# Kernel tuning notes

Measured on AMD Instinct MI355X. Metric: run time of the kernel, lower is better.

The kernel has to match this reference:

```python
import jax, jax.numpy as jnp
import numpy as np

D_MODEL = 1024
N_HEADS = 16
D_K = D_MODEL // N_HEADS


def setup_inputs() -> dict:
    key = jax.random.key(0)
    ks = jax.random.split(key, 9)
    s = 1.0 / np.sqrt(D_MODEL)
    inp = {
        "x": jax.random.normal(ks[0], (2, 2048, D_MODEL), dtype=jnp.float32),
        "wq": jax.random.uniform(ks[1], (D_MODEL, D_MODEL), jnp.float32, -s, s),
        "bq": jax.random.uniform(ks[2], (D_MODEL,), jnp.float32, -s, s),
        "wk": jax.random.uniform(ks[3], (D_MODEL, D_MODEL), jnp.float32, -s, s),
        "bk": jax.random.uniform(ks[4], (D_MODEL,), jnp.float32, -s, s),
        "wv": jax.random.uniform(ks[5], (D_MODEL, D_MODEL), jnp.float32, -s, s),
        "bv": jax.random.uniform(ks[6], (D_MODEL,), jnp.float32, -s, s),
        "wo": jax.random.uniform(ks[7], (D_MODEL, D_MODEL), jnp.float32, -s, s),
        "bo": jax.random.uniform(ks[8], (D_MODEL,), jnp.float32, -s, s),
    }
    return inp


def reference(x, wq, bq, wk, bk, wv, bv, wo, bo):
    B, S, _ = x.shape
    # projections; weights stored as [in, out] (torch Linear applies x @ W^T; here W pre-transposed)
    def proj(w, b):
        y = x @ w + b  # [B,S,D]
        return y.reshape(B, S, N_HEADS, D_K).transpose(0, 2, 1, 3)  # [B,H,S,dk]
    q, k, v = proj(wq, bq), proj(wk, bk), proj(wv, bv)
    scores = jnp.einsum('bhqd,bhkd->bhqk', q, k) / jnp.sqrt(jnp.float32(D_K))
    attn = jax.nn.softmax(scores, axis=-1)  # dropout p=0 -> identity
    ctx = jnp.einsum('bhqk,bhkd->bhqd', attn, v)
    ctx = ctx.transpose(0, 2, 1, 3).reshape(B, S, D_MODEL)
    return ctx @ wo + bo
```

## Files before the change

### kernel.cpp

```cpp
#include <hip/hip_runtime.h>
#include <hip/hip_bf16.h>
#include <math.h>


typedef __attribute__((ext_vector_type(8))) short bf8v;
typedef __attribute__((ext_vector_type(4))) float f32x4;
typedef __attribute__((ext_vector_type(16))) float f32x16;

#define mfma32(a, b, c) __builtin_amdgcn_mfma_f32_32x32x16_bf16((a), (b), (c), 0, 0, 0)

constexpr int Dm = 1024;
constexpr int NH = 16;
constexpr int DK = 64;
constexpr int BB = 2;
constexpr int SS = 2048;
constexpr int MM = BB * SS;

__device__ __forceinline__ unsigned short f2bf(float f) {
  union { float f; unsigned u; } v; v.f = f;
  unsigned r = v.u + 0x7fffu + ((v.u >> 16) & 1u);
  return (unsigned short)(r >> 16);
}

__device__ __forceinline__ unsigned cvt_pk_bf16(float lo, float hi) {
  unsigned r;
  asm("v_cvt_pk_bf16_f32 %0, %1, %2" : "=v"(r) : "v"(lo), "v"(hi));
  return r;
}

__device__ __forceinline__ void swap32(unsigned &a, unsigned &b) {
  asm("v_permlane32_swap_b32 %0, %1" : "+v"(a), "+v"(b));
}

__device__ __forceinline__ void gl_lds16(const void* g, void* l) {
  __builtin_amdgcn_global_load_lds(
      (const __attribute__((address_space(1))) void*)g,
      (__attribute__((address_space(3))) void*)l, 16, 0, 0);
}

__device__ __forceinline__ int swz4(int r) { return (r ^ (r >> 2)) & 3; }
__device__ __forceinline__ bf8v frag4(const unsigned short* base, int R, int s0) {
  return *(const bf8v*)((const char*)base + R * 64 + ((s0 ^ swz4(R)) << 4));
}
__device__ __forceinline__ bf8v rd8(const unsigned short* base, int row, int slot) {
  return *(const bf8v*)((const char*)base + row * 128 + (((slot ^ row) & 7) << 4));
}

__global__ __launch_bounds__(256) void transw_kernel(
    const float* __restrict__ w0, const float* __restrict__ w1,
    const float* __restrict__ w2, const float* __restrict__ w3,
    unsigned short* __restrict__ dstBase)
{
  const float* src = (blockIdx.y == 0) ? w0 : (blockIdx.y == 1) ? w1
                   : (blockIdx.y == 2) ? w2 : w3;
  unsigned short* dst = dstBase + (size_t)blockIdx.y * (Dm * Dm);
  int idx = blockIdx.x * 256 + threadIdx.x;
  int i = idx & (Dm - 1);
  int o = (idx >> 10) << 2;
  float4 v = *(const float4*)(src + (size_t)i * Dm + o);
  dst[(size_t)(o + 0) * Dm + i] = f2bf(v.x);
  dst[(size_t)(o + 1) * Dm + i] = f2bf(v.y);
  dst[(size_t)(o + 2) * Dm + i] = f2bf(v.z);
  dst[(size_t)(o + 3) * Dm + i] = f2bf(v.w);
}

__global__ __launch_bounds__(256) void proj_kernel(
    const float* __restrict__ x, const unsigned short* __restrict__ WtBase,
    const float* __restrict__ bq, const float* __restrict__ bk, const float* __restrict__ bv,
    unsigned short* __restrict__ Qh, unsigned short* __restrict__ Kh,
    unsigned short* __restrict__ Vh)
{
  __shared__ unsigned short As[2][128 * 32];
  __shared__ unsigned short Bs[2][128 * 32];
  const int z = blockIdx.z;
  const unsigned short* W = WtBase + (size_t)z * (Dm * Dm);
  const float* bias = (z == 0) ? bq : (z == 1) ? bk : bv;

  const int tid = threadIdx.x, lane = tid & 63, wave = tid >> 6;
  const int wm = wave >> 1, wn = wave & 1;
  const int m0 = blockIdx.y * 128, n0 = blockIdx.x * 128;
  const int l15 = lane & 15, l4 = lane >> 4;

  const int q1 = tid, q2 = tid + 256;
  const int rw1 = q1 >> 2, sl1 = q1 & 3, c1 = sl1 ^ swz4(rw1);
  const int rw2 = q2 >> 2, sl2 = q2 & 3, c2 = sl2 ^ swz4(rw2);
  const int ldsOff1 = (q1 - lane) * 16, ldsOff2 = (q2 - lane) * 16;

  f32x4 acc[4][4] = {};
  float4 a1, a1b, a2, a2b;

  auto loadA = [&](int k0) {
    const float* s1 = x + (size_t)(m0 + rw1) * Dm + k0 + c1 * 8;
    const float* s2 = x + (size_t)(m0 + rw2) * Dm + k0 + c2 * 8;
    a1 = *(const float4*)s1; a1b = *(const float4*)(s1 + 4);
    a2 = *(const float4*)s2; a2b = *(const float4*)(s2 + 4);
  };
  auto stageB = [&](int buf, int k0) {
    gl_lds16(W + (size_t)(n0 + rw1) * Dm + k0 + c1 * 8, (char*)Bs[buf] + ldsOff1);
    gl_lds16(W + (size_t)(n0 + rw2) * Dm + k0 + c2 * 8, (char*)Bs[buf] + ldsOff2);
  };
  auto writeA = [&](int buf) {
    bf8v v;
    v[0] = (short)f2bf(a1.x);  v[1] = (short)f2bf(a1.y);
    v[2] = (short)f2bf(a1.z);  v[3] = (short)f2bf(a1.w);
    v[4] = (short)f2bf(a1b.x); v[5] = (short)f2bf(a1b.y);
    v[6] = (short)f2bf(a1b.z); v[7] = (short)f2bf(a1b.w);
    *(bf8v*)((char*)As[buf] + rw1 * 64 + (sl1 << 4)) = v;
    v[0] = (short)f2bf(a2.x);  v[1] = (short)f2bf(a2.y);
    v[2] = (short)f2bf(a2.z);  v[3] = (short)f2bf(a2.w);
    v[4] = (short)f2bf(a2b.x); v[5] = (short)f2bf(a2b.y);
    v[6] = (short)f2bf(a2b.z); v[7] = (short)f2bf(a2b.w);
    *(bf8v*)((char*)As[buf] + rw2 * 64 + (sl2 << 4)) = v;
  };

  loadA(0);
  stageB(0, 0);
  writeA(0);
  __syncthreads();

  for (int k0 = 0; k0 < Dm; k0 += 32) {
    const int cur = (k0 >> 5) & 1, nxt = cur ^ 1;
    const bool more = (k0 + 32) < Dm;
    if (more) { loadA(k0 + 32); stageB(nxt, k0 + 32); }

    bf8v af[4], bfr[4];
    #pragma unroll
    for (int i = 0; i < 4; ++i) af[i] = frag4(As[cur], wm * 64 + i * 16 + l15, l4);
    #pragma unroll
    for (int j = 0; j < 4; ++j) bfr[j] = frag4(Bs[cur], wn * 64 + j * 16 + l15, l4);
    __builtin_amdgcn_s_setprio(1);
    #pragma unroll
    for (int i = 0; i < 4; ++i)
      #pragma unroll
      for (int j = 0; j < 4; ++j)
        acc[i][j] = __builtin_amdgcn_mfma_f32_16x16x32_bf16(af[i], bfr[j], acc[i][j], 0, 0, 0);
    __builtin_amdgcn_s_setprio(0);

    if (more) writeA(nxt);
    __syncthreads();
  }

  unsigned short* Out = (z == 0) ? Qh : (z == 1) ? Kh : Vh;
  const float oscale = (z == 0) ? 0.18033688011112042f : 1.0f;
  #pragma unroll
  for (int i = 0; i < 4; ++i)
    #pragma unroll
    for (int j = 0; j < 4; ++j) {
      int row = m0 + wm * 64 + i * 16 + l4 * 4;
      int col = n0 + wn * 64 + j * 16 + l15;
      float bcol = bias[col];
      int h = col >> 6, d = col & 63;
      #pragma unroll
      for (int r = 0; r < 4; ++r) {
        int rr = row + r;
        int b = rr >> 11, s = rr & 2047;
        unsigned short val = f2bf((acc[i][j][r] + bcol) * oscale);
        if (z < 2)
          Out[(((size_t)(b * NH + h) * SS + s) * DK) + d] = val;
        else
          Out[((size_t)(b * NH + h) * DK + d) * SS + s] = val;
      }
    }
}

__global__ __launch_bounds__(256) void outproj_kernel(
    const unsigned short* __restrict__ Ctx, const unsigned short* __restrict__ Wto,
    const float* __restrict__ bo, float* __restrict__ Out)
{
  __shared__ unsigned short As[2][128 * 32];
  __shared__ unsigned short Bs[2][128 * 32];
  const int tid = threadIdx.x, lane = tid & 63, wave = tid >> 6;
  const int wm = wave >> 1, wn = wave & 1;
  const int m0 = blockIdx.y * 128, n0 = blockIdx.x * 128;
  const int l15 = lane & 15, l4 = lane >> 4;

  const int q1 = tid, q2 = tid + 256;
  const int rw1 = q1 >> 2, sl1 = q1 & 3, c1 = sl1 ^ swz4(rw1);
  const int rw2 = q2 >> 2, sl2 = q2 & 3, c2 = sl2 ^ swz4(rw2);
  const int ldsOff1 = (q1 - lane) * 16, ldsOff2 = (q2 - lane) * 16;

  auto srcA = [&](int rw, int c, int k0) -> const unsigned short* {
    int rr = m0 + rw, b = rr >> 11, s = rr & 2047;
    int col = k0 + c * 8, h = col >> 6, d = col & 63;
    return Ctx + ((size_t)(b * NH + h) * SS + s) * DK + d;
  };
  auto stageAB = [&](int buf, int k0) {
    gl_lds16(srcA(rw1, c1, k0), (char*)As[buf] + ldsOff1);
    gl_lds16(srcA(rw2, c2, k0), (char*)As[buf] + ldsOff2);
    gl_lds16(Wto + (size_t)(n0 + rw1) * Dm + k0 + c1 * 8, (char*)Bs[buf] + ldsOff1);
    gl_lds16(Wto + (size_t)(n0 + rw2) * Dm + k0 + c2 * 8, (char*)Bs[buf] + ldsOff2);
  };

  f32x4 acc[4][4] = {};

  stageAB(0, 0);
  __syncthreads();

  for (int k0 = 0; k0 < Dm; k0 += 32) {
    const int cur = (k0 >> 5) & 1, nxt = cur ^ 1;
    if (k0 + 32 < Dm) stageAB(nxt, k0 + 32);

    bf8v af[4], bfr[4];
    #pragma unroll
    for (int i = 0; i < 4; ++i) af[i] = frag4(As[cur], wm * 64 + i * 16 + l15, l4);
    #pragma unroll
    for (int j = 0; j < 4; ++j) bfr[j] = frag4(Bs[cur], wn * 64 + j * 16 + l15, l4);
    __builtin_amdgcn_s_setprio(1);
    #pragma unroll
    for (int i = 0; i < 4; ++i)
      #pragma unroll
      for (int j = 0; j < 4; ++j)
        acc[i][j] = __builtin_amdgcn_mfma_f32_16x16x32_bf16(af[i], bfr[j], acc[i][j], 0, 0, 0);
    __builtin_amdgcn_s_setprio(0);
    __syncthreads();
  }

  #pragma unroll
  for (int i = 0; i < 4; ++i)
    #pragma unroll
    for (int j = 0; j < 4; ++j) {
      int row = m0 + wm * 64 + i * 16 + l4 * 4;
      int col = n0 + wn * 64 + j * 16 + l15;
      float bcol = bo[col];
      #pragma unroll
      for (int r = 0; r < 4; ++r)
        Out[(size_t)(row + r) * Dm + col] = acc[i][j][r] + bcol;
    }
}

__global__ __launch_bounds__(512, 4) void attn_kernel(
    const unsigned short* __restrict__ Q, const unsigned short* __restrict__ K,
    const unsigned short* __restrict__ Vt, unsigned short* __restrict__ CtxQ)
{
  __shared__ __align__(16) unsigned short smem[32768];
  unsigned short* KlB = smem;
  unsigned short* VlB = smem + 16384;

  const int tid = threadIdx.x, lane = tid & 63, wave = tid >> 6;
  const int qsub = wave & 3, khalf = wave >> 2;
  const int l31 = lane & 31, hi = lane >> 5;
  const int bh = blockIdx.y;
  const int q0 = blockIdx.x * 128 + qsub * 32;
  const size_t base = (size_t)bh * SS * DK;

  bf8v qf[4];
  #pragma unroll
  for (int dc = 0; dc < 4; ++dc)
    qf[dc] = *(const bf8v*)(Q + base + (size_t)(q0 + l31) * DK + dc * 16 + hi * 8);

  float m = -INFINITY, lpart = 0.f;
  f32x16 cacc[2] = {};

  const int srow = tid >> 3, ssl = tid & 7, sc = ssl ^ (srow & 7);
  const int soff = (tid - lane) * 16;
  auto kslab = [&](int buf, int h) { return KlB + (buf * 2 + h) * 4096; };
  auto vslab = [&](int buf, int h) { return VlB + (buf * 2 + h) * 4096; };
  auto stage = [&](int buf, int kt) {
    gl_lds16(K + base + (size_t)(kt + srow) * DK + sc * 8,          (char*)kslab(buf, 0) + soff);
    gl_lds16(K + base + (size_t)(1024 + kt + srow) * DK + sc * 8,   (char*)kslab(buf, 1) + soff);
    gl_lds16(Vt + base + (size_t)srow * SS + kt + sc * 8,           (char*)vslab(buf, 0) + soff);
    gl_lds16(Vt + base + (size_t)srow * SS + 1024 + kt + sc * 8,    (char*)vslab(buf, 1) + soff);
  };

  constexpr int NT = 16;
  stage(0, 0);
  __syncthreads();

  for (int t = 0; t < NT; ++t) {
    const int cur = t & 1;
    if (t + 1 < NT) stage(cur ^ 1, (t + 1) * 64);
    const unsigned short* Kb = kslab(cur, khalf);
    const unsigned short* Vb = vslab(cur, khalf);

    f32x16 st0 = {}, st1 = {};
    __builtin_amdgcn_s_setprio(1);
    #pragma unroll
    for (int dc = 0; dc < 4; ++dc) {
      bf8v kf0 = rd8(Kb, l31, dc * 2 + hi);
      bf8v kf1 = rd8(Kb, 32 + l31, dc * 2 + hi);
      st0 = mfma32(kf0, qf[dc], st0);
      st1 = mfma32(kf1, qf[dc], st1);
    }
    __builtin_amdgcn_s_setprio(0);

    float mx = -INFINITY;
    #pragma unroll
    for (int r = 0; r < 16; ++r) mx = fmaxf(mx, fmaxf(st0[r], st1[r]));
    mx = fmaxf(mx, __shfl_xor(mx, 1));
    mx = fmaxf(mx, __shfl_xor(mx, 2));
    mx = fmaxf(mx, __shfl_xor(mx, 4));
    mx = fmaxf(mx, __shfl_xor(mx, 8));
    mx = fmaxf(mx, __shfl_xor(mx, 16));
    mx = fmaxf(mx, __shfl_xor(mx, 32));

    if (mx - m > 8.0f) {
      float alpha = exp2f(m - mx);
      m = mx;
      lpart *= alpha;
      #pragma unroll
      for (int n = 0; n < 2; ++n)
        #pragma unroll
        for (int r = 0; r < 16; ++r) cacc[n][r] *= alpha;
    }

    auto process = [&](const f32x16& st, int ktile) {
      float p[16];
      #pragma unroll
      for (int r = 0; r < 16; ++r) p[r] = exp2f(st[r] - m);
      float sA = ((p[0] + p[1]) + (p[2] + p[3])) + ((p[4] + p[5]) + (p[6] + p[7]));
      float sB = ((p[8] + p[9]) + (p[10] + p[11])) + ((p[12] + p[13]) + (p[14] + p[15]));
      lpart += sA + sB;
      #pragma unroll
      for (int c = 0; c < 2; ++c) {
        const int o = c * 8;
        unsigned A  = cvt_pk_bf16(p[o + 0], p[o + 1]);
        unsigned B  = cvt_pk_bf16(p[o + 4], p[o + 5]);
        unsigned Cw = cvt_pk_bf16(p[o + 2], p[o + 3]);
        unsigned Dw = cvt_pk_bf16(p[o + 6], p[o + 7]);
        swap32(A, B); swap32(Cw, Dw);
        union { bf8v v; unsigned w[4]; } pf;
        pf.w[0] = A; pf.w[1] = Cw; pf.w[2] = B; pf.w[3] = Dw;
        const int slot = ktile * 4 + c * 2 + hi;
        bf8v vb0 = rd8(Vb, l31, slot);
        bf8v vb1 = rd8(Vb, 32 + l31, slot);
        __builtin_amdgcn_s_setprio(1);
        cacc[0] = mfma32(vb0, pf.v, cacc[0]);
        cacc[1] = mfma32(vb1, pf.v, cacc[1]);
        __builtin_amdgcn_s_setprio(0);
      }
    };
    process(st0, 0);
    process(st1, 1);

    __syncthreads();
  }

  float lf = lpart + __shfl_xor(lpart, 32);
  float* scr = (float*)smem;
  float* fs = scr + qsub * 2176;

  if (khalf == 1) {
    #pragma unroll
    for (int n = 0; n < 2; ++n)
      #pragma unroll
      for (int r = 0; r < 16; ++r)
        fs[(n * 16 + r) * 64 + lane] = cacc[n][r];
    fs[2048 + lane] = lf;
    if (lane == 0) fs[2048 + 64] = m;
  }
  __syncthreads();
  if (khalf == 0) {
    float mB = fs[2048 + 64];
    float lB = fs[2048 + lane];
    float mt = fmaxf(m, mB);
    float a  = exp2f(m - mt), b2 = exp2f(mB - mt);
    float inv = 1.0f / (lf * a + lB * b2);
    float fa = a * inv, fb = b2 * inv;
    #pragma unroll
    for (int n = 0; n < 2; ++n)
      #pragma unroll
      for (int j = 0; j < 4; ++j) {
        float v0 = cacc[n][4 * j + 0] * fa + fs[(n * 16 + 4 * j + 0) * 64 + lane] * fb;
        float v1 = cacc[n][4 * j + 1] * fa + fs[(n * 16 + 4 * j + 1) * 64 + lane] * fb;
        float v2 = cacc[n][4 * j + 2] * fa + fs[(n * 16 + 4 * j + 2) * 64 + lane] * fb;
        float v3 = cacc[n][4 * j + 3] * fa + fs[(n * 16 + 4 * j + 3) * 64 + lane] * fb;
        uint2 w;
        w.x = cvt_pk_bf16(v0, v1);
        w.y = cvt_pk_bf16(v2, v3);
        int d = n * 32 + 8 * j + 4 * hi;
        *(uint2*)(CtxQ + base + (size_t)(q0 + l31) * DK + d) = w;
      }
  }
}

extern "C" void kernel_launch(void* const* d_in, const int* in_sizes, int n_in,
                              void* d_out, int out_size, void* d_ws, size_t ws_size,
                              hipStream_t stream) {
  const float* x  = (const float*)d_in[0];
  const float* wq = (const float*)d_in[1];
  const float* bq = (const float*)d_in[2];
  const float* wk = (const float*)d_in[3];
  const float* bk = (const float*)d_in[4];
  const float* wv = (const float*)d_in[5];
  const float* bv = (const float*)d_in[6];
  const float* wo = (const float*)d_in[7];
  const float* bo = (const float*)d_in[8];
  float* out = (float*)d_out;

  unsigned short* ws = (unsigned short*)d_ws;
  const size_t WPLANE = (size_t)Dm * Dm;
  const size_t PLANE  = (size_t)MM * Dm;
  unsigned short* Wt  = ws;
  unsigned short* Qh  = ws + PLANE;
  unsigned short* Kh  = ws + 2 * PLANE;
  unsigned short* Vh  = ws + 3 * PLANE;
  unsigned short* Wto = Wt + 3 * WPLANE;

  transw_kernel<<<dim3(1024, 4), dim3(256), 0, stream>>>(wq, wk, wv, wo, Wt);
  proj_kernel<<<dim3(Dm / 128, MM / 128, 3), dim3(256), 0, stream>>>(
      x, Wt, bq, bk, bv, Qh, Kh, Vh);
  attn_kernel<<<dim3(SS / 128, BB * NH), dim3(512), 0, stream>>>(Qh, Kh, Vh, Qh);
  outproj_kernel<<<dim3(Dm / 128, MM / 128), dim3(256), 0, stream>>>(Qh, Wto, bo, out);
}
```

Measured before the change: 151.2 us.

## Split attention KV tiles across wave halves and shrink LDS for higher occupancy

The attention kernel previously had each wave half handle a separate half of the key sequence, with two 64-key subtiles per iteration. Now both halves share one 64-key tile per iteration, each wave taking 32 keys. This halves the LDS footprint and score registers, and launch bounds rise from 4 to 6 blocks per SM. The GEMM A-tile conversion also switches to packed bf16 conversion. The trade-off is twice as many loop iterations and barriers for the same work.

```diff
diff --git a/kernel.cpp b/kernel.cpp
--- a/kernel.cpp
+++ b/kernel.cpp
@@ -100,17 +100,13 @@
     gl_lds16(W + (size_t)(n0 + rw2) * Dm + k0 + c2 * 8, (char*)Bs[buf] + ldsOff2);
   };
   auto writeA = [&](int buf) {
-    bf8v v;
-    v[0] = (short)f2bf(a1.x);  v[1] = (short)f2bf(a1.y);
-    v[2] = (short)f2bf(a1.z);  v[3] = (short)f2bf(a1.w);
-    v[4] = (short)f2bf(a1b.x); v[5] = (short)f2bf(a1b.y);
-    v[6] = (short)f2bf(a1b.z); v[7] = (short)f2bf(a1b.w);
-    *(bf8v*)((char*)As[buf] + rw1 * 64 + (sl1 << 4)) = v;
-    v[0] = (short)f2bf(a2.x);  v[1] = (short)f2bf(a2.y);
-    v[2] = (short)f2bf(a2.z);  v[3] = (short)f2bf(a2.w);
-    v[4] = (short)f2bf(a2b.x); v[5] = (short)f2bf(a2b.y);
-    v[6] = (short)f2bf(a2b.z); v[7] = (short)f2bf(a2b.w);
-    *(bf8v*)((char*)As[buf] + rw2 * 64 + (sl2 << 4)) = v;
+    union { bf8v v; unsigned w[4]; } u;
+    u.w[0] = cvt_pk_bf16(a1.x,  a1.y);  u.w[1] = cvt_pk_bf16(a1.z,  a1.w);
+    u.w[2] = cvt_pk_bf16(a1b.x, a1b.y); u.w[3] = cvt_pk_bf16(a1b.z, a1b.w);
+    *(bf8v*)((char*)As[buf] + rw1 * 64 + (sl1 << 4)) = u.v;
+    u.w[0] = cvt_pk_bf16(a2.x,  a2.y);  u.w[1] = cvt_pk_bf16(a2.z,  a2.w);
+    u.w[2] = cvt_pk_bf16(a2b.x, a2b.y); u.w[3] = cvt_pk_bf16(a2b.z, a2b.w);
+    *(bf8v*)((char*)As[buf] + rw2 * 64 + (sl2 << 4)) = u.v;
   };
 
   loadA(0);
@@ -228,13 +224,13 @@
     }
 }
 
-__global__ __launch_bounds__(512, 4) void attn_kernel(
+__global__ __launch_bounds__(512, 6) void attn_kernel(
     const unsigned short* __restrict__ Q, const unsigned short* __restrict__ K,
     const unsigned short* __restrict__ Vt, unsigned short* __restrict__ CtxQ)
 {
-  __shared__ __align__(16) unsigned short smem[32768];
+  __shared__ __align__(16) unsigned short smem[17408];
   unsigned short* KlB = smem;
-  unsigned short* VlB = smem + 16384;
+  unsigned short* VlB = smem + 8192;
 
   const int tid = threadIdx.x, lane = tid & 63, wave = tid >> 6;
   const int qsub = wave & 3, khalf = wave >> 2;
@@ -253,39 +249,37 @@
 
   const int srow = tid >> 3, ssl = tid & 7, sc = ssl ^ (srow & 7);
   const int soff = (tid - lane) * 16;
-  auto kslab = [&](int buf, int h) { return KlB + (buf * 2 + h) * 4096; };
-  auto vslab = [&](int buf, int h) { return VlB + (buf * 2 + h) * 4096; };
+  auto kslab = [&](int buf) { return KlB + buf * 4096; };
+  auto vslab = [&](int buf) { return VlB + buf * 4096; };
   auto stage = [&](int buf, int kt) {
-    gl_lds16(K + base + (size_t)(kt + srow) * DK + sc * 8,          (char*)kslab(buf, 0) + soff);
-    gl_lds16(K + base + (size_t)(1024 + kt + srow) * DK + sc * 8,   (char*)kslab(buf, 1) + soff);
-    gl_lds16(Vt + base + (size_t)srow * SS + kt + sc * 8,           (char*)vslab(buf, 0) + soff);
-    gl_lds16(Vt + base + (size_t)srow * SS + 1024 + kt + sc * 8,    (char*)vslab(buf, 1) + soff);
-  };
-
-  constexpr int NT = 16;
+    gl_lds16(K + base + (size_t)(kt + srow) * DK + sc * 8, (char*)kslab(buf) + soff);
+    gl_lds16(Vt + base + (size_t)srow * SS + kt + sc * 8,  (char*)vslab(buf) + soff);
+  };
+
+  constexpr int NT = SS / 64;
   stage(0, 0);
   __syncthreads();
 
   for (int t = 0; t < NT; ++t) {
     const int cur = t & 1;
     if (t + 1 < NT) stage(cur ^ 1, (t + 1) * 64);
-    const unsigned short* Kb = kslab(cur, khalf);
-    const unsigned short* Vb = vslab(cur, khalf);
-
-    f32x16 st0 = {}, st1 = {};
+    const unsigned short* Kb = kslab(cur);
+    const unsigned short* Vb = vslab(cur);
+
+    f32x16 st = {};
     __builtin_amdgcn_s_setprio(1);
     #pragma unroll
     for (int dc = 0; dc < 4; ++dc) {
-      bf8v kf0 = rd8(Kb, l31, dc * 2 + hi);
-      bf8v kf1 = rd8(Kb, 32 + l31, dc * 2 + hi);
-      st0 = mfma32(kf0, qf[dc], st0);
-      st1 = mfma32(kf1, qf[dc], st1);
+      bf8v kf = rd8(Kb, khalf * 32 + l31, dc * 2 + hi);
+      st = mfma32(kf, qf[dc], st);
     }
     __builtin_amdgcn_s_setprio(0);
 
-    float mx = -INFINITY;
-    #pragma unroll
-    for (int r = 0; r < 16; ++r) mx = fmaxf(mx, fmaxf(st0[r], st1[r]));
+    float m0a = fmaxf(fmaxf(st[0], st[1]),  fmaxf(st[2], st[3]));
+    float m0b = fmaxf(fmaxf(st[4], st[5]),  fmaxf(st[6], st[7]));
+    float m0c = fmaxf(fmaxf(st[8], st[9]),  fmaxf(st[10], st[11]));
+    float m0d = fmaxf(fmaxf(st[12], st[13]), fmaxf(st[14], st[15]));
+    float mx = fmaxf(fmaxf(m0a, m0b), fmaxf(m0c, m0d));
     mx = fmaxf(mx, __shfl_xor(mx, 1));
     mx = fmaxf(mx, __shfl_xor(mx, 2));
     mx = fmaxf(mx, __shfl_xor(mx, 4));
@@ -303,34 +297,29 @@
         for (int r = 0; r < 16; ++r) cacc[n][r] *= alpha;
     }
 
-    auto process = [&](const f32x16& st, int ktile) {
-      float p[16];
-      #pragma unroll
-      for (int r = 0; r < 16; ++r) p[r] = exp2f(st[r] - m);
-      float sA = ((p[0] + p[1]) + (p[2] + p[3])) + ((p[4] + p[5]) + (p[6] + p[7]));
-      float sB = ((p[8] + p[9]) + (p[10] + p[11])) + ((p[12] + p[13]) + (p[14] + p[15]));
-      lpart += sA + sB;
-      #pragma unroll
-      for (int c = 0; c < 2; ++c) {
-        const int o = c * 8;
-        unsigned A  = cvt_pk_bf16(p[o + 0], p[o + 1]);
-        unsigned B  = cvt_pk_bf16(p[o + 4], p[o + 5]);
-        unsigned Cw = cvt_pk_bf16(p[o + 2], p[o + 3]);
-        unsigned Dw = cvt_pk_bf16(p[o + 6], p[o + 7]);
-        swap32(A, B); swap32(Cw, Dw);
-        union { bf8v v; unsigned w[4]; } pf;
-        pf.w[0] = A; pf.w[1] = Cw; pf.w[2] = B; pf.w[3] = Dw;
-        const int slot = ktile * 4 + c * 2 + hi;
-        bf8v vb0 = rd8(Vb, l31, slot);
-        bf8v vb1 = rd8(Vb, 32 + l31, slot);
-        __builtin_amdgcn_s_setprio(1);
-        cacc[0] = mfma32(vb0, pf.v, cacc[0]);
-        cacc[1] = mfma32(vb1, pf.v, cacc[1]);
-        __builtin_amdgcn_s_setprio(0);
-      }
-    };
-    process(st0, 0);
-    process(st1, 1);
+    float p[16];
+    #pragma unroll
+    for (int r = 0; r < 16; ++r) p[r] = exp2f(st[r] - m);
+    lpart += (((p[0] + p[1]) + (p[2] + p[3])) + ((p[4] + p[5]) + (p[6] + p[7])))
+           + (((p[8] + p[9]) + (p[10] + p[11])) + ((p[12] + p[13]) + (p[14] + p[15])));
+    #pragma unroll
+    for (int c = 0; c < 2; ++c) {
+      const int o = c * 8;
+      unsigned A  = cvt_pk_bf16(p[o + 0], p[o + 1]);
+      unsigned B  = cvt_pk_bf16(p[o + 4], p[o + 5]);
+      unsigned Cw = cvt_pk_bf16(p[o + 2], p[o + 3]);
+      unsigned Dw = cvt_pk_bf16(p[o + 6], p[o + 7]);
+      swap32(A, B); swap32(Cw, Dw);
+      union { bf8v v; unsigned w[4]; } pf;
+      pf.w[0] = A; pf.w[1] = Cw; pf.w[2] = B; pf.w[3] = Dw;
+      const int slot = khalf * 4 + c * 2 + hi;
+      bf8v vb0 = rd8(Vb, l31, slot);
+      bf8v vb1 = rd8(Vb, 32 + l31, slot);
+      __builtin_amdgcn_s_setprio(1);
+      cacc[0] = mfma32(vb0, pf.v, cacc[0]);
+      cacc[1] = mfma32(vb1, pf.v, cacc[1]);
+      __builtin_amdgcn_s_setprio(0);
+    }
 
     __syncthreads();
   }
```

Measured after the change: 234.9 us. 55.4% more time.

## Use per-row softmax max and MFMA row-sum; pack bf16 conversion in projection

Applied to the files above, without the earlier changes.

The attention kernel now keeps a separate running max for each query row instead of one max per wave, which drops the cross-lane shuffle reduction. The row-sum is computed by an extra MFMA against a ones vector rather than by scalar adds, and each row's max is stored to LDS for the final merge of the two key halves. The projection's A-tile conversion uses packed bf16 converts in place of per-element rounding. This trims VALU and shuffle work but adds one MFMA per PV step and a per-row rescale decision.

```diff
diff --git a/kernel.cpp b/kernel.cpp
--- a/kernel.cpp
+++ b/kernel.cpp
@@ -100,17 +100,13 @@
     gl_lds16(W + (size_t)(n0 + rw2) * Dm + k0 + c2 * 8, (char*)Bs[buf] + ldsOff2);
   };
   auto writeA = [&](int buf) {
-    bf8v v;
-    v[0] = (short)f2bf(a1.x);  v[1] = (short)f2bf(a1.y);
-    v[2] = (short)f2bf(a1.z);  v[3] = (short)f2bf(a1.w);
-    v[4] = (short)f2bf(a1b.x); v[5] = (short)f2bf(a1b.y);
-    v[6] = (short)f2bf(a1b.z); v[7] = (short)f2bf(a1b.w);
-    *(bf8v*)((char*)As[buf] + rw1 * 64 + (sl1 << 4)) = v;
-    v[0] = (short)f2bf(a2.x);  v[1] = (short)f2bf(a2.y);
-    v[2] = (short)f2bf(a2.z);  v[3] = (short)f2bf(a2.w);
-    v[4] = (short)f2bf(a2b.x); v[5] = (short)f2bf(a2b.y);
-    v[6] = (short)f2bf(a2b.z); v[7] = (short)f2bf(a2b.w);
-    *(bf8v*)((char*)As[buf] + rw2 * 64 + (sl2 << 4)) = v;
+    union { bf8v v; unsigned w[4]; } u;
+    u.w[0] = cvt_pk_bf16(a1.x,  a1.y);  u.w[1] = cvt_pk_bf16(a1.z,  a1.w);
+    u.w[2] = cvt_pk_bf16(a1b.x, a1b.y); u.w[3] = cvt_pk_bf16(a1b.z, a1b.w);
+    *(bf8v*)((char*)As[buf] + rw1 * 64 + (sl1 << 4)) = u.v;
+    u.w[0] = cvt_pk_bf16(a2.x,  a2.y);  u.w[1] = cvt_pk_bf16(a2.z,  a2.w);
+    u.w[2] = cvt_pk_bf16(a2b.x, a2b.y); u.w[3] = cvt_pk_bf16(a2b.z, a2b.w);
+    *(bf8v*)((char*)As[buf] + rw2 * 64 + (sl2 << 4)) = u.v;
   };
 
   loadA(0);
@@ -248,8 +244,13 @@
   for (int dc = 0; dc < 4; ++dc)
     qf[dc] = *(const bf8v*)(Q + base + (size_t)(q0 + l31) * DK + dc * 16 + hi * 8);
 
-  float m = -INFINITY, lpart = 0.f;
+  bf8v onesv;
+  #pragma unroll
+  for (int e = 0; e < 8; ++e) onesv[e] = (short)0x3F80;
+
+  float m = -INFINITY;
   f32x16 cacc[2] = {};
+  f32x16 lacc = {};
 
   const int srow = tid >> 3, ssl = tid & 7, sc = ssl ^ (srow & 7);
   const int soff = (tid - lane) * 16;
@@ -283,20 +284,20 @@
     }
     __builtin_amdgcn_s_setprio(0);
 
-    float mx = -INFINITY;
-    #pragma unroll
-    for (int r = 0; r < 16; ++r) mx = fmaxf(mx, fmaxf(st0[r], st1[r]));
-    mx = fmaxf(mx, __shfl_xor(mx, 1));
-    mx = fmaxf(mx, __shfl_xor(mx, 2));
-    mx = fmaxf(mx, __shfl_xor(mx, 4));
-    mx = fmaxf(mx, __shfl_xor(mx, 8));
-    mx = fmaxf(mx, __shfl_xor(mx, 16));
+    float a8[8];
+    #pragma unroll
+    for (int r = 0; r < 8; ++r)
+      a8[r] = fmaxf(fmaxf(st0[2 * r], st0[2 * r + 1]),
+                    fmaxf(st1[2 * r], st1[2 * r + 1]));
+    float mx = fmaxf(fmaxf(fmaxf(a8[0], a8[1]), fmaxf(a8[2], a8[3])),
+                     fmaxf(fmaxf(a8[4], a8[5]), fmaxf(a8[6], a8[7])));
     mx = fmaxf(mx, __shfl_xor(mx, 32));
 
-    if (mx - m > 8.0f) {
-      float alpha = exp2f(m - mx);
-      m = mx;
-      lpart *= alpha;
+    if (!__all((mx - m <= 8.0f) ? 1 : 0)) {
+      float mnew = fmaxf(m, mx);
+      float alpha = exp2f(m - mnew);
+      m = mnew;
+      lacc[0] *= alpha;
       #pragma unroll
       for (int n = 0; n < 2; ++n)
         #pragma unroll
@@ -307,9 +308,6 @@
       float p[16];
       #pragma unroll
       for (int r = 0; r < 16; ++r) p[r] = exp2f(st[r] - m);
-      float sA = ((p[0] + p[1]) + (p[2] + p[3])) + ((p[4] + p[5]) + (p[6] + p[7]));
-      float sB = ((p[8] + p[9]) + (p[10] + p[11])) + ((p[12] + p[13]) + (p[14] + p[15]));
-      lpart += sA + sB;
       #pragma unroll
       for (int c = 0; c < 2; ++c) {
         const int o = c * 8;
@@ -326,6 +324,7 @@
         __builtin_amdgcn_s_setprio(1);
         cacc[0] = mfma32(vb0, pf.v, cacc[0]);
         cacc[1] = mfma32(vb1, pf.v, cacc[1]);
+        lacc    = mfma32(onesv, pf.v, lacc);
         __builtin_amdgcn_s_setprio(0);
       }
     };
@@ -335,7 +334,7 @@
     __syncthreads();
   }
 
-  float lf = lpart + __shfl_xor(lpart, 32);
+  float lf = lacc[0];
   float* scr = (float*)smem;
   float* fs = scr + qsub * 2176;
 
@@ -346,11 +345,11 @@
       for (int r = 0; r < 16; ++r)
         fs[(n * 16 + r) * 64 + lane] = cacc[n][r];
     fs[2048 + lane] = lf;
-    if (lane == 0) fs[2048 + 64] = m;
+    fs[2112 + lane] = m;
   }
   __syncthreads();
   if (khalf == 0) {
-    float mB = fs[2048 + 64];
+    float mB = fs[2112 + lane];
     float lB = fs[2048 + lane];
     float mt = fmaxf(m, mB);
     float a  = exp2f(m - mt), b2 = exp2f(mB - mt);
```

After: 144.0 us. 4.8% less time.
